# Performance work log

Measured on AMD Instinct MI355X. Metric: run time of the kernel, lower is better.

## Reference

```python
import jax, jax.numpy as jnp
import numpy as np

B, T, IN, H, OUT, L = 64, 4096, 32, 128, 32, 2


def setup_inputs() -> dict:
    key = jax.random.key(0)
    ks = jax.random.split(key, 12)
    s = 1.0 / np.sqrt(H)
    inp = {"x": jax.random.normal(ks[0], (B, T, IN), dtype=jnp.float32)}
    # layer 0 (input_dim -> H), layer 1 (H -> H); PyTorch GRU layout: [3H, in] with gates (r, z, n)
    inp["W_ih0"] = jax.random.uniform(ks[1], (3 * H, IN), jnp.float32, -s, s)
    inp["W_hh0"] = jax.random.uniform(ks[2], (3 * H, H), jnp.float32, -s, s)
    inp["b_ih0"] = jax.random.uniform(ks[3], (3 * H,), jnp.float32, -s, s)
    inp["b_hh0"] = jax.random.uniform(ks[4], (3 * H,), jnp.float32, -s, s)
    inp["W_ih1"] = jax.random.uniform(ks[5], (3 * H, H), jnp.float32, -s, s)
    inp["W_hh1"] = jax.random.uniform(ks[6], (3 * H, H), jnp.float32, -s, s)
    inp["b_ih1"] = jax.random.uniform(ks[7], (3 * H,), jnp.float32, -s, s)
    inp["b_hh1"] = jax.random.uniform(ks[8], (3 * H,), jnp.float32, -s, s)
    inp["fc_w"] = jax.random.uniform(ks[9], (OUT, H), jnp.float32, -s, s)
    inp["fc_b"] = jax.random.uniform(ks[10], (OUT,), jnp.float32, -s, s)
    return inp


def _gru_layer(x_seq, W_ih, W_hh, b_ih, b_hh):
    # x_seq: [B, T, in]; precompute the input projection as one big GEMM
    gi = jnp.einsum("bti,gi->btg", x_seq, W_ih) + b_ih  # [B, T, 3H]
    h0 = jnp.zeros((x_seq.shape[0], W_hh.shape[1]), x_seq.dtype)

    def step(h, gi_t):
        gh = h @ W_hh.T + b_hh  # [B, 3H]
        i_r, i_z, i_n = jnp.split(gi_t, 3, axis=-1)
        h_r, h_z, h_n = jnp.split(gh, 3, axis=-1)
        r = jax.nn.sigmoid(i_r + h_r)
        z = jax.nn.sigmoid(i_z + h_z)
        n = jnp.tanh(i_n + r * h_n)
        h_new = (1.0 - z) * n + z * h
        return h_new, h_new

    hT, outs = jax.lax.scan(step, h0, jnp.swapaxes(gi, 0, 1))  # outs: [T, B, H]
    return jnp.swapaxes(outs, 0, 1), hT


def reference(x, W_ih0, W_hh0, b_ih0, b_hh0, W_ih1, W_hh1, b_ih1, b_hh1, fc_w, fc_b):
    y0, h0 = _gru_layer(x, W_ih0, W_hh0, b_ih0, b_hh0)
    y1, h1 = _gru_layer(y0, W_ih1, W_hh1, b_ih1, b_hh1)
    out = jnp.einsum("bth,oh->bto", y1, fc_w) + fc_b  # [B, T, OUT]
    h = jnp.stack([h0, h1], axis=0)  # [n_layers, B, H]
    return out, h
```

## Files before the change

kernel.cpp:

```cpp
#include <hip/hip_runtime.h>

#define BB 64
#define TT 4096
#define IN0 32
#define HH 128
#define G3 384
#define NOUT 32
#define RING 64
#define CH 8

typedef _Float16 h2 __attribute__((ext_vector_type(2)));
typedef _Float16 h8 __attribute__((ext_vector_type(8)));
union H8 { h8 v; h2 p[4]; };

struct SM {
    float pg[G3 * 5];
    float pgi[G3 * 5];
    float hs[2][HH];
    _Float16 hf[2][HH];
    _Float16 xh[2][IN0];
    _Float16 ys[CH][HH];
    float bias1[G3];
    float bias2[G3];
    float fcw[NOUT * 129];
    float fcb[NOUT];
    float pfc[NOUT * 9];
};

__device__ __forceinline__ float fast_sigmoid(float x) {
    x = fminf(fmaxf(x, -30.f), 30.f);
    float e = __expf(-x);
    return __builtin_amdgcn_rcpf(1.f + e);
}
__device__ __forceinline__ float fast_tanh(float x) {
    x = fminf(fmaxf(x, -15.f), 15.f);
    float e = __expf(-2.f * x);
    return (1.f - e) * __builtin_amdgcn_rcpf(1.f + e);
}
__device__ __forceinline__ float fdot2(h2 a, h2 b, float c) {
#if __has_builtin(__builtin_amdgcn_fdot2)
    return __builtin_amdgcn_fdot2(a, b, c, false);
#else
    return fmaf((float)a.x, (float)b.x, fmaf((float)a.y, (float)b.y, c));
#endif
}
__device__ __forceinline__ int aload(const int* p) {
    return __hip_atomic_load(p, __ATOMIC_RELAXED, __HIP_MEMORY_SCOPE_AGENT);
}
__device__ __forceinline__ void astore(int* p, int v) {
    __hip_atomic_store(p, v, __ATOMIC_RELAXED, __HIP_MEMORY_SCOPE_AGENT);
}
__device__ __forceinline__ h2 cvt2(float a, float b) {
    h2 r; r.x = (_Float16)a; r.y = (_Float16)b; return r;
}

__device__ void role_A(SM& sm, const float* __restrict__ xb,
                       const float* __restrict__ W_ih, const float* __restrict__ W_hh,
                       const float* __restrict__ b_ih, const float* __restrict__ b_hh,
                       _Float16* __restrict__ y0b, float* __restrict__ hout, int* flagA)
{
    const int tid = threadIdx.x;
    const int rp = tid % 192, kq = tid / 192;
    const int r0 = 2 * rp, r1 = r0 + 1;
    const int pA0 = r0 * 5 + kq, pA1 = r1 * 5 + kq;

    h2 wh0[16], wh1[16], wi0[4], wi1[4];
    #pragma unroll
    for (int i = 0; i < 16; ++i) {
        float2 f0 = *(const float2*)&W_hh[r0 * HH + kq * 32 + 2 * i];
        float2 f1 = *(const float2*)&W_hh[r1 * HH + kq * 32 + 2 * i];
        wh0[i] = cvt2(f0.x, f0.y); wh1[i] = cvt2(f1.x, f1.y);
    }
    #pragma unroll
    for (int i = 0; i < 4; ++i) {
        float2 f0 = *(const float2*)&W_ih[r0 * IN0 + kq * 8 + 2 * i];
        float2 f1 = *(const float2*)&W_ih[r1 * IN0 + kq * 8 + 2 * i];
        wi0[i] = cvt2(f0.x, f0.y); wi1[i] = cvt2(f1.x, f1.y);
    }
    for (int i = tid; i < G3; i += 768) { sm.bias1[i] = b_ih[i]; sm.bias2[i] = b_hh[i]; }
    if (tid < HH) { sm.hs[0][tid] = 0.f; sm.hf[0][tid] = (_Float16)0.f; }
    if (tid < 8) {
        float4 f = ((const float4*)xb)[tid];
        ((h2*)&sm.xh[0][0])[2 * tid]     = cvt2(f.x, f.y);
        ((h2*)&sm.xh[0][0])[2 * tid + 1] = cvt2(f.z, f.w);
    }
    __syncthreads();

    int cur = 0;
    for (int t = 0; t < TT; ++t) {
        float4 pf;
        if (tid >= 128 && tid < 136) {
            int tn = (t + 1 < TT) ? t + 1 : t;
            pf = ((const float4*)(xb + (size_t)tn * IN0))[tid - 128];
        }
        const h8* hv = (const h8*)&sm.hf[cur][kq * 32];
        float a0 = 0.f, a1 = 0.f;
        #pragma unroll
        for (int i = 0; i < 4; ++i) {
            H8 hh; hh.v = hv[i];
            #pragma unroll
            for (int j = 0; j < 4; ++j) {
                a0 = fdot2(wh0[4 * i + j], hh.p[j], a0);
                a1 = fdot2(wh1[4 * i + j], hh.p[j], a1);
            }
        }
        sm.pg[pA0] = a0; sm.pg[pA1] = a1;
        H8 xx; xx.v = ((const h8*)&sm.xh[cur][0])[kq];
        float c0 = 0.f, c1 = 0.f;
        #pragma unroll
        for (int j = 0; j < 4; ++j) {
            c0 = fdot2(wi0[j], xx.p[j], c0);
            c1 = fdot2(wi1[j], xx.p[j], c1);
        }
        sm.pgi[pA0] = c0; sm.pgi[pA1] = c1;
        __syncthreads();

        const int nxt = cur ^ 1;
        if (tid < HH) {
            const int j = tid;
            float gir = sm.pgi[j*5+0]+sm.pgi[j*5+1]+sm.pgi[j*5+2]+sm.pgi[j*5+3] + sm.bias1[j];
            float giz = sm.pgi[(j+HH)*5+0]+sm.pgi[(j+HH)*5+1]+sm.pgi[(j+HH)*5+2]+sm.pgi[(j+HH)*5+3] + sm.bias1[j+HH];
            float gin = sm.pgi[(j+2*HH)*5+0]+sm.pgi[(j+2*HH)*5+1]+sm.pgi[(j+2*HH)*5+2]+sm.pgi[(j+2*HH)*5+3] + sm.bias1[j+2*HH];
            float ghr = sm.pg[j*5+0]+sm.pg[j*5+1]+sm.pg[j*5+2]+sm.pg[j*5+3] + sm.bias2[j];
            float ghz = sm.pg[(j+HH)*5+0]+sm.pg[(j+HH)*5+1]+sm.pg[(j+HH)*5+2]+sm.pg[(j+HH)*5+3] + sm.bias2[j+HH];
            float ghn = sm.pg[(j+2*HH)*5+0]+sm.pg[(j+2*HH)*5+1]+sm.pg[(j+2*HH)*5+2]+sm.pg[(j+2*HH)*5+3] + sm.bias2[j+2*HH];
            float rg = fast_sigmoid(gir + ghr);
            float zg = fast_sigmoid(giz + ghz);
            float ng = fast_tanh(gin + rg * ghn);
            float hn = (1.f - zg) * ng + zg * sm.hs[cur][j];
            sm.hs[nxt][j] = hn;
            sm.hf[nxt][j] = (_Float16)hn;
            y0b[(size_t)t * HH + j] = (_Float16)hn;
            if (t == TT - 1) hout[j] = hn;
        } else if (tid < 136) {
            int i = tid - 128;
            ((h2*)&sm.xh[nxt][0])[2 * i]     = cvt2(pf.x, pf.y);
            ((h2*)&sm.xh[nxt][0])[2 * i + 1] = cvt2(pf.z, pf.w);
        }
        __syncthreads();
        if ((t & 7) == 7 && tid == 0) { __threadfence(); astore(flagA, t + 1); }
        cur = nxt;
    }
}

__device__ void role_B(SM& sm, const _Float16* __restrict__ y0b,
                       const float* __restrict__ W_ih, const float* __restrict__ b_ih,
                       float* __restrict__ ring, int* flagA, int* flagB, int* flagC)
{
    const int tid = threadIdx.x;
    const int rp = tid % 192, kq = tid / 192;
    const int r0 = 2 * rp, r1 = r0 + 1;
    const int pA0 = r0 * 5 + kq, pA1 = r1 * 5 + kq;

    h2 wi0[16], wi1[16];
    #pragma unroll
    for (int i = 0; i < 16; ++i) {
        float2 f0 = *(const float2*)&W_ih[r0 * HH + kq * 32 + 2 * i];
        float2 f1 = *(const float2*)&W_ih[r1 * HH + kq * 32 + 2 * i];
        wi0[i] = cvt2(f0.x, f0.y); wi1[i] = cvt2(f1.x, f1.y);
    }
    for (int i = tid; i < G3; i += 768) sm.bias1[i] = b_ih[i];

    for (int T0 = 0; T0 < TT; T0 += CH) {
        if (tid == 0) {
            while (aload(flagA) < T0 + CH) __builtin_amdgcn_s_sleep(2);
            int need = T0 + CH - RING;
            while (aload(flagC) < need) __builtin_amdgcn_s_sleep(2);
            __threadfence();
        }
        __syncthreads();
        for (int i = tid; i < CH * HH / 2; i += 768)
            ((unsigned*)sm.ys)[i] = ((const unsigned*)(y0b + (size_t)T0 * HH))[i];
        __syncthreads();
        for (int s = 0; s < CH; ++s) {
            const h8* yv = (const h8*)&sm.ys[s][kq * 32];
            float a0 = 0.f, a1 = 0.f;
            #pragma unroll
            for (int i = 0; i < 4; ++i) {
                H8 yy; yy.v = yv[i];
                #pragma unroll
                for (int j = 0; j < 4; ++j) {
                    a0 = fdot2(wi0[4 * i + j], yy.p[j], a0);
                    a1 = fdot2(wi1[4 * i + j], yy.p[j], a1);
                }
            }
            sm.pg[pA0] = a0; sm.pg[pA1] = a1;
            __syncthreads();
            if (tid < G3) {
                float sum = sm.pg[tid*5+0]+sm.pg[tid*5+1]+sm.pg[tid*5+2]+sm.pg[tid*5+3] + sm.bias1[tid];
                ring[(size_t)((T0 + s) & (RING - 1)) * G3 + tid] = sum;
            }
            __syncthreads();
        }
        if (tid == 0) { __threadfence(); astore(flagB, T0 + CH); }
    }
}

__device__ void role_C(SM& sm, const float* __restrict__ ring,
                       const float* __restrict__ W_hh, const float* __restrict__ b_hh,
                       const float* __restrict__ fc_w, const float* __restrict__ fc_b,
                       float* __restrict__ outb, float* __restrict__ hout,
                       int* flagB, int* flagC)
{
    const int tid = threadIdx.x;
    const int rp = tid % 192, kq = tid / 192;
    const int r0 = 2 * rp, r1 = r0 + 1;
    const int pA0 = r0 * 5 + kq, pA1 = r1 * 5 + kq;

    h2 wh0[16], wh1[16];
    #pragma unroll
    for (int i = 0; i < 16; ++i) {
        float2 f0 = *(const float2*)&W_hh[r0 * HH + kq * 32 + 2 * i];
        float2 f1 = *(const float2*)&W_hh[r1 * HH + kq * 32 + 2 * i];
        wh0[i] = cvt2(f0.x, f0.y); wh1[i] = cvt2(f1.x, f1.y);
    }
    if (tid == 0) astore(flagC, 0);
    for (int i = tid; i < G3; i += 768) sm.bias2[i] = b_hh[i];
    for (int i = tid; i < NOUT * HH; i += 768)
        sm.fcw[(i >> 7) * 129 + (i & 127)] = fc_w[i];
    if (tid < NOUT) sm.fcb[tid] = fc_b[tid];
    if (tid < HH) { sm.hs[0][tid] = 0.f; sm.hf[0][tid] = (_Float16)0.f; }
    __syncthreads();

    int cur = 0;
    for (int t = 0; t < TT; ++t) {
        if ((t & 7) == 0) {
            if (tid == 0) {
                while (aload(flagB) < t + CH) __builtin_amdgcn_s_sleep(2);
                __threadfence();
            }
            __syncthreads();
        }
        if (t >= 2 && tid >= 704 && tid < 736) {
            int o = tid - 704;
            float s = sm.fcb[o];
            #pragma unroll
            for (int j = 0; j < 8; ++j) s += sm.pfc[o * 9 + j];
            outb[(size_t)(t - 2) * NOUT + o] = s;
        }
        float gir = 0.f, giz = 0.f, gin = 0.f;
        if (tid < HH) {
            const float* rr = ring + (size_t)(t & (RING - 1)) * G3;
            gir = rr[tid]; giz = rr[tid + HH]; gin = rr[tid + 2 * HH];
        }
        const h8* hv = (const h8*)&sm.hf[cur][kq * 32];
        float a0 = 0.f, a1 = 0.f;
        #pragma unroll
        for (int i = 0; i < 4; ++i) {
            H8 hh; hh.v = hv[i];
            #pragma unroll
            for (int j = 0; j < 4; ++j) {
                a0 = fdot2(wh0[4 * i + j], hh.p[j], a0);
                a1 = fdot2(wh1[4 * i + j], hh.p[j], a1);
            }
        }
        sm.pg[pA0] = a0; sm.pg[pA1] = a1;
        __syncthreads();

        const int nxt = cur ^ 1;
        if (tid < HH) {
            const int j = tid;
            float ghr = sm.pg[j*5+0]+sm.pg[j*5+1]+sm.pg[j*5+2]+sm.pg[j*5+3] + sm.bias2[j];
            float ghz = sm.pg[(j+HH)*5+0]+sm.pg[(j+HH)*5+1]+sm.pg[(j+HH)*5+2]+sm.pg[(j+HH)*5+3] + sm.bias2[j+HH];
            float ghn = sm.pg[(j+2*HH)*5+0]+sm.pg[(j+2*HH)*5+1]+sm.pg[(j+2*HH)*5+2]+sm.pg[(j+2*HH)*5+3] + sm.bias2[j+2*HH];
            float rg = fast_sigmoid(gir + ghr);
            float zg = fast_sigmoid(giz + ghz);
            float ng = fast_tanh(gin + rg * ghn);
            float hn = (1.f - zg) * ng + zg * sm.hs[cur][j];
            sm.hs[nxt][j] = hn;
            sm.hf[nxt][j] = (_Float16)hn;
            if (t == TT - 1) hout[j] = hn;
        }
        if (tid >= 384 && tid < 640) {
            int idx = tid - 384, o = idx & 31, ks = idx >> 5;
            const float* hv2 = &sm.hs[cur][ks * 16];
            const float* wv = &sm.fcw[o * 129 + ks * 16];
            float s = 0.f;
            #pragma unroll
            for (int i = 0; i < 16; ++i) s = fmaf(hv2[i], wv[i], s);
            sm.pfc[o * 9 + ks] = s;
        }
        __syncthreads();
        if ((t & 7) == 7 && tid == 0) { __threadfence(); astore(flagC, t + 1); }
        cur = nxt;
    }
    if (tid >= 704 && tid < 736) {
        int o = tid - 704;
        float s = sm.fcb[o];
        #pragma unroll
        for (int j = 0; j < 8; ++j) s += sm.pfc[o * 9 + j];
        outb[(size_t)(TT - 2) * NOUT + o] = s;
    }
    __syncthreads();
    if (tid >= 384 && tid < 640) {
        int idx = tid - 384, o = idx & 31, ks = idx >> 5;
        const float* hv2 = &sm.hs[cur][ks * 16];
        const float* wv = &sm.fcw[o * 129 + ks * 16];
        float s = 0.f;
        #pragma unroll
        for (int i = 0; i < 16; ++i) s = fmaf(hv2[i], wv[i], s);
        sm.pfc[o * 9 + ks] = s;
    }
    __syncthreads();
    if (tid >= 704 && tid < 736) {
        int o = tid - 704;
        float s = sm.fcb[o];
        #pragma unroll
        for (int j = 0; j < 8; ++j) s += sm.pfc[o * 9 + j];
        outb[(size_t)(TT - 1) * NOUT + o] = s;
    }
}

extern "C" __global__ void __launch_bounds__(768, 3)
gru_pipe_kernel(
    const float* x,
    const float* W_ih0, const float* W_hh0, const float* b_ih0, const float* b_hh0,
    const float* W_ih1, const float* W_hh1, const float* b_ih1, const float* b_hh1,
    const float* fc_w, const float* fc_b,
    float* out, float* hstack, _Float16* y0, float* ring, int* flags)
{
    __shared__ SM sm;
    const int wg = blockIdx.x;
    if (wg < BB) {
        const int b = wg;
        role_A(sm, x + (size_t)b * TT * IN0, W_ih0, W_hh0, b_ih0, b_hh0,
               y0 + (size_t)b * TT * HH, hstack + b * HH,
               &flags[(0 * 64 + b) * 16]);
    } else if (wg < 2 * BB) {
        const int b = wg - BB;
        role_B(sm, y0 + (size_t)b * TT * HH, W_ih1, b_ih1,
               ring + (size_t)b * RING * G3,
               &flags[(0 * 64 + b) * 16], &flags[(1 * 64 + b) * 16], &flags[(2 * 64 + b) * 16]);
    } else {
        const int b = wg - 2 * BB;
        role_C(sm, ring + (size_t)b * RING * G3, W_hh1, b_hh1, fc_w, fc_b,
               out + (size_t)b * TT * NOUT, hstack + BB * HH + b * HH,
               &flags[(1 * 64 + b) * 16], &flags[(2 * 64 + b) * 16]);
    }
}

extern "C" void kernel_launch(void* const* d_in, const int* in_sizes, int n_in,
                              void* d_out, int out_size, void* d_ws, size_t ws_size,
                              hipStream_t stream) {
    const float* x     = (const float*)d_in[0];
    const float* W_ih0 = (const float*)d_in[1];
    const float* W_hh0 = (const float*)d_in[2];
    const float* b_ih0 = (const float*)d_in[3];
    const float* b_hh0 = (const float*)d_in[4];
    const float* W_ih1 = (const float*)d_in[5];
    const float* W_hh1 = (const float*)d_in[6];
    const float* b_ih1 = (const float*)d_in[7];
    const float* b_hh1 = (const float*)d_in[8];
    const float* fc_w  = (const float*)d_in[9];
    const float* fc_b  = (const float*)d_in[10];

    float* out    = (float*)d_out;
    float* hstack = out + (size_t)BB * TT * NOUT;
    _Float16* y0  = (_Float16*)d_ws;
    float* ring   = (float*)((char*)d_ws + (68ull << 20));
    int* flags    = (int*)((char*)d_ws + (80ull << 20));

    gru_pipe_kernel<<<3 * BB, 768, 0, stream>>>(
        x, W_ih0, W_hh0, b_ih0, b_hh0,
        W_ih1, W_hh1, b_ih1, b_hh1,
        fc_w, fc_b, out, hstack, y0, ring, flags);
}
```

Baseline: 4.901 ms.

## Fuse both GRU layers and FC into one workgroup per batch with wavefront-skewed steps

Replaces the three-role inter-workgroup pipeline, which passed data through global memory with flag spin-waits, with a single workgroup per batch element. That workgroup runs layer 0, layer 1 and the FC projection skewed by one timestep each. Partial dot products are reduced across the four k-quarter lanes with DPP moves instead of shared-memory partial arrays, and x is prefetched in chunks of 16 steps. This removes the global y0 and ring traffic and the flag polling, but each thread now holds roughly three times as many weight registers and the workgroup does more work per step.

Result: slower. 5.779 ms (+17.9%).

```diff
diff --git a/kernel.cpp b/kernel.cpp
--- a/kernel.cpp
+++ b/kernel.cpp
@@ -6,22 +6,22 @@
 #define HH 128
 #define G3 384
 #define NOUT 32
-#define RING 64
-#define CH 8
+#define CHX 16
 
 typedef _Float16 h2 __attribute__((ext_vector_type(2)));
 typedef _Float16 h8 __attribute__((ext_vector_type(8)));
 union H8 { h8 v; h2 p[4]; };
 
 struct SM {
-    float pg[G3 * 5];
-    float pgi[G3 * 5];
-    float hs[2][HH];
-    _Float16 hf[2][HH];
-    _Float16 xh[2][IN0];
-    _Float16 ys[CH][HH];
-    float bias1[G3];
-    float bias2[G3];
+    float g0h[G3];
+    float g0i[G3];
+    float g1h[G3];
+    float g1i[G3];
+    float hs0[2][HH];
+    float hs1[2][HH];
+    _Float16 hf0[2][HH];
+    _Float16 hf1[2][HH];
+    _Float16 xh[2][CHX][IN0];
     float fcw[NOUT * 129];
     float fcb[NOUT];
     float pfc[NOUT * 9];
@@ -44,298 +44,174 @@
     return fmaf((float)a.x, (float)b.x, fmaf((float)a.y, (float)b.y, c));
 #endif
 }
-__device__ __forceinline__ int aload(const int* p) {
-    return __hip_atomic_load(p, __ATOMIC_RELAXED, __HIP_MEMORY_SCOPE_AGENT);
-}
-__device__ __forceinline__ void astore(int* p, int v) {
-    __hip_atomic_store(p, v, __ATOMIC_RELAXED, __HIP_MEMORY_SCOPE_AGENT);
-}
 __device__ __forceinline__ h2 cvt2(float a, float b) {
     h2 r; r.x = (_Float16)a; r.y = (_Float16)b; return r;
 }
-
-__device__ void role_A(SM& sm, const float* __restrict__ xb,
-                       const float* __restrict__ W_ih, const float* __restrict__ W_hh,
-                       const float* __restrict__ b_ih, const float* __restrict__ b_hh,
-                       _Float16* __restrict__ y0b, float* __restrict__ hout, int* flagA)
+__device__ __forceinline__ float qxor1(float v) {
+    return __int_as_float(__builtin_amdgcn_mov_dpp(__float_as_int(v), 0xB1, 0xF, 0xF, true));
+}
+__device__ __forceinline__ float qxor2(float v) {
+    return __int_as_float(__builtin_amdgcn_mov_dpp(__float_as_int(v), 0x4E, 0xF, 0xF, true));
+}
+
+extern "C" __global__ void __launch_bounds__(768, 3)
+gru_fused_kernel(
+    const float* __restrict__ x,
+    const float* __restrict__ W_ih0, const float* __restrict__ W_hh0,
+    const float* __restrict__ b_ih0, const float* __restrict__ b_hh0,
+    const float* __restrict__ W_ih1, const float* __restrict__ W_hh1,
+    const float* __restrict__ b_ih1, const float* __restrict__ b_hh1,
+    const float* __restrict__ fc_w, const float* __restrict__ fc_b,
+    float* __restrict__ out, float* __restrict__ hstack)
 {
+    __shared__ SM sm;
+    const int b = blockIdx.x;
     const int tid = threadIdx.x;
-    const int rp = tid % 192, kq = tid / 192;
+    const int rp = tid >> 2, kq = tid & 3;
     const int r0 = 2 * rp, r1 = r0 + 1;
-    const int pA0 = r0 * 5 + kq, pA1 = r1 * 5 + kq;
-
-    h2 wh0[16], wh1[16], wi0[4], wi1[4];
+    const float* xb = x + (size_t)b * TT * IN0;
+    float* outb = out + (size_t)b * TT * NOUT;
+
+    h2 wh0[32], wh1[32], wi1[32], wi0[8];
     #pragma unroll
     for (int i = 0; i < 16; ++i) {
-        float2 f0 = *(const float2*)&W_hh[r0 * HH + kq * 32 + 2 * i];
-        float2 f1 = *(const float2*)&W_hh[r1 * HH + kq * 32 + 2 * i];
-        wh0[i] = cvt2(f0.x, f0.y); wh1[i] = cvt2(f1.x, f1.y);
+        float2 f;
+        f = *(const float2*)&W_hh0[r0*HH + kq*32 + 2*i]; wh0[i]    = cvt2(f.x, f.y);
+        f = *(const float2*)&W_hh0[r1*HH + kq*32 + 2*i]; wh0[16+i] = cvt2(f.x, f.y);
+        f = *(const float2*)&W_hh1[r0*HH + kq*32 + 2*i]; wh1[i]    = cvt2(f.x, f.y);
+        f = *(const float2*)&W_hh1[r1*HH + kq*32 + 2*i]; wh1[16+i] = cvt2(f.x, f.y);
+        f = *(const float2*)&W_ih1[r0*HH + kq*32 + 2*i]; wi1[i]    = cvt2(f.x, f.y);
+        f = *(const float2*)&W_ih1[r1*HH + kq*32 + 2*i]; wi1[16+i] = cvt2(f.x, f.y);
     }
     #pragma unroll
     for (int i = 0; i < 4; ++i) {
-        float2 f0 = *(const float2*)&W_ih[r0 * IN0 + kq * 8 + 2 * i];
-        float2 f1 = *(const float2*)&W_ih[r1 * IN0 + kq * 8 + 2 * i];
-        wi0[i] = cvt2(f0.x, f0.y); wi1[i] = cvt2(f1.x, f1.y);
-    }
-    for (int i = tid; i < G3; i += 768) { sm.bias1[i] = b_ih[i]; sm.bias2[i] = b_hh[i]; }
-    if (tid < HH) { sm.hs[0][tid] = 0.f; sm.hf[0][tid] = (_Float16)0.f; }
-    if (tid < 8) {
-        float4 f = ((const float4*)xb)[tid];
-        ((h2*)&sm.xh[0][0])[2 * tid]     = cvt2(f.x, f.y);
-        ((h2*)&sm.xh[0][0])[2 * tid + 1] = cvt2(f.z, f.w);
-    }
-    __syncthreads();
-
-    int cur = 0;
-    for (int t = 0; t < TT; ++t) {
-        float4 pf;
-        if (tid >= 128 && tid < 136) {
-            int tn = (t + 1 < TT) ? t + 1 : t;
-            pf = ((const float4*)(xb + (size_t)tn * IN0))[tid - 128];
-        }
-        const h8* hv = (const h8*)&sm.hf[cur][kq * 32];
-        float a0 = 0.f, a1 = 0.f;
-        #pragma unroll
-        for (int i = 0; i < 4; ++i) {
-            H8 hh; hh.v = hv[i];
-            #pragma unroll
-            for (int j = 0; j < 4; ++j) {
-                a0 = fdot2(wh0[4 * i + j], hh.p[j], a0);
-                a1 = fdot2(wh1[4 * i + j], hh.p[j], a1);
-            }
-        }
-        sm.pg[pA0] = a0; sm.pg[pA1] = a1;
-        H8 xx; xx.v = ((const h8*)&sm.xh[cur][0])[kq];
-        float c0 = 0.f, c1 = 0.f;
-        #pragma unroll
-        for (int j = 0; j < 4; ++j) {
-            c0 = fdot2(wi0[j], xx.p[j], c0);
-            c1 = fdot2(wi1[j], xx.p[j], c1);
-        }
-        sm.pgi[pA0] = c0; sm.pgi[pA1] = c1;
-        __syncthreads();
-
-        const int nxt = cur ^ 1;
-        if (tid < HH) {
-            const int j = tid;
-            float gir = sm.pgi[j*5+0]+sm.pgi[j*5+1]+sm.pgi[j*5+2]+sm.pgi[j*5+3] + sm.bias1[j];
-            float giz = sm.pgi[(j+HH)*5+0]+sm.pgi[(j+HH)*5+1]+sm.pgi[(j+HH)*5+2]+sm.pgi[(j+HH)*5+3] + sm.bias1[j+HH];
-            float gin = sm.pgi[(j+2*HH)*5+0]+sm.pgi[(j+2*HH)*5+1]+sm.pgi[(j+2*HH)*5+2]+sm.pgi[(j+2*HH)*5+3] + sm.bias1[j+2*HH];
-            float ghr = sm.pg[j*5+0]+sm.pg[j*5+1]+sm.pg[j*5+2]+sm.pg[j*5+3] + sm.bias2[j];
-            float ghz = sm.pg[(j+HH)*5+0]+sm.pg[(j+HH)*5+1]+sm.pg[(j+HH)*5+2]+sm.pg[(j+HH)*5+3] + sm.bias2[j+HH];
-            float ghn = sm.pg[(j+2*HH)*5+0]+sm.pg[(j+2*HH)*5+1]+sm.pg[(j+2*HH)*5+2]+sm.pg[(j+2*HH)*5+3] + sm.bias2[j+2*HH];
-            float rg = fast_sigmoid(gir + ghr);
-            float zg = fast_sigmoid(giz + ghz);
-            float ng = fast_tanh(gin + rg * ghn);
-            float hn = (1.f - zg) * ng + zg * sm.hs[cur][j];
-            sm.hs[nxt][j] = hn;
-            sm.hf[nxt][j] = (_Float16)hn;
-            y0b[(size_t)t * HH + j] = (_Float16)hn;
-            if (t == TT - 1) hout[j] = hn;
-        } else if (tid < 136) {
-            int i = tid - 128;
-            ((h2*)&sm.xh[nxt][0])[2 * i]     = cvt2(pf.x, pf.y);
-            ((h2*)&sm.xh[nxt][0])[2 * i + 1] = cvt2(pf.z, pf.w);
-        }
-        __syncthreads();
-        if ((t & 7) == 7 && tid == 0) { __threadfence(); astore(flagA, t + 1); }
-        cur = nxt;
-    }
-}
-
-__device__ void role_B(SM& sm, const _Float16* __restrict__ y0b,
-                       const float* __restrict__ W_ih, const float* __restrict__ b_ih,
-                       float* __restrict__ ring, int* flagA, int* flagB, int* flagC)
-{
-    const int tid = threadIdx.x;
-    const int rp = tid % 192, kq = tid / 192;
-    const int r0 = 2 * rp, r1 = r0 + 1;
-    const int pA0 = r0 * 5 + kq, pA1 = r1 * 5 + kq;
-
-    h2 wi0[16], wi1[16];
-    #pragma unroll
-    for (int i = 0; i < 16; ++i) {
-        float2 f0 = *(const float2*)&W_ih[r0 * HH + kq * 32 + 2 * i];
-        float2 f1 = *(const float2*)&W_ih[r1 * HH + kq * 32 + 2 * i];
-        wi0[i] = cvt2(f0.x, f0.y); wi1[i] = cvt2(f1.x, f1.y);
-    }
-    for (int i = tid; i < G3; i += 768) sm.bias1[i] = b_ih[i];
-
-    for (int T0 = 0; T0 < TT; T0 += CH) {
-        if (tid == 0) {
-            while (aload(flagA) < T0 + CH) __builtin_amdgcn_s_sleep(2);
-            int need = T0 + CH - RING;
-            while (aload(flagC) < need) __builtin_amdgcn_s_sleep(2);
-            __threadfence();
-        }
-        __syncthreads();
-        for (int i = tid; i < CH * HH / 2; i += 768)
-            ((unsigned*)sm.ys)[i] = ((const unsigned*)(y0b + (size_t)T0 * HH))[i];
-        __syncthreads();
-        for (int s = 0; s < CH; ++s) {
-            const h8* yv = (const h8*)&sm.ys[s][kq * 32];
-            float a0 = 0.f, a1 = 0.f;
-            #pragma unroll
-            for (int i = 0; i < 4; ++i) {
-                H8 yy; yy.v = yv[i];
-                #pragma unroll
-                for (int j = 0; j < 4; ++j) {
-                    a0 = fdot2(wi0[4 * i + j], yy.p[j], a0);
-                    a1 = fdot2(wi1[4 * i + j], yy.p[j], a1);
-                }
-            }
-            sm.pg[pA0] = a0; sm.pg[pA1] = a1;
-            __syncthreads();
-            if (tid < G3) {
-                float sum = sm.pg[tid*5+0]+sm.pg[tid*5+1]+sm.pg[tid*5+2]+sm.pg[tid*5+3] + sm.bias1[tid];
-                ring[(size_t)((T0 + s) & (RING - 1)) * G3 + tid] = sum;
-            }
-            __syncthreads();
-        }
-        if (tid == 0) { __threadfence(); astore(flagB, T0 + CH); }
-    }
-}
-
-__device__ void role_C(SM& sm, const float* __restrict__ ring,
-                       const float* __restrict__ W_hh, const float* __restrict__ b_hh,
-                       const float* __restrict__ fc_w, const float* __restrict__ fc_b,
-                       float* __restrict__ outb, float* __restrict__ hout,
-                       int* flagB, int* flagC)
-{
-    const int tid = threadIdx.x;
-    const int rp = tid % 192, kq = tid / 192;
-    const int r0 = 2 * rp, r1 = r0 + 1;
-    const int pA0 = r0 * 5 + kq, pA1 = r1 * 5 + kq;
-
-    h2 wh0[16], wh1[16];
-    #pragma unroll
-    for (int i = 0; i < 16; ++i) {
-        float2 f0 = *(const float2*)&W_hh[r0 * HH + kq * 32 + 2 * i];
-        float2 f1 = *(const float2*)&W_hh[r1 * HH + kq * 32 + 2 * i];
-        wh0[i] = cvt2(f0.x, f0.y); wh1[i] = cvt2(f1.x, f1.y);
-    }
-    if (tid == 0) astore(flagC, 0);
-    for (int i = tid; i < G3; i += 768) sm.bias2[i] = b_hh[i];
+        float2 f;
+        f = *(const float2*)&W_ih0[r0*IN0 + kq*8 + 2*i]; wi0[i]   = cvt2(f.x, f.y);
+        f = *(const float2*)&W_ih0[r1*IN0 + kq*8 + 2*i]; wi0[4+i] = cvt2(f.x, f.y);
+    }
+    const bool lead = (kq == 0);
+    const float bh0a = lead ? b_hh0[r0] : 0.f, bh0b = lead ? b_hh0[r1] : 0.f;
+    const float bh1a = lead ? b_hh1[r0] : 0.f, bh1b = lead ? b_hh1[r1] : 0.f;
+    const float bi1a = lead ? b_ih1[r0] : 0.f, bi1b = lead ? b_ih1[r1] : 0.f;
+    const float bi0a = lead ? b_ih0[r0] : 0.f, bi0b = lead ? b_ih0[r1] : 0.f;
+
+    if (tid < HH) {
+        sm.hs0[0][tid] = 0.f; sm.hs0[1][tid] = 0.f;
+        sm.hs1[0][tid] = 0.f; sm.hs1[1][tid] = 0.f;
+        sm.hf0[0][tid] = (_Float16)0.f; sm.hf0[1][tid] = (_Float16)0.f;
+        sm.hf1[0][tid] = (_Float16)0.f; sm.hf1[1][tid] = (_Float16)0.f;
+    }
     for (int i = tid; i < NOUT * HH; i += 768)
         sm.fcw[(i >> 7) * 129 + (i & 127)] = fc_w[i];
     if (tid < NOUT) sm.fcb[tid] = fc_b[tid];
-    if (tid < HH) { sm.hs[0][tid] = 0.f; sm.hf[0][tid] = (_Float16)0.f; }
+    if (tid >= 640) {
+        int i = tid - 640;
+        float4 f = ((const float4*)xb)[i];
+        ((h2*)&sm.xh[0][0][0])[2*i]   = cvt2(f.x, f.y);
+        ((h2*)&sm.xh[0][0][0])[2*i+1] = cvt2(f.z, f.w);
+    }
     __syncthreads();
 
     int cur = 0;
-    for (int t = 0; t < TT; ++t) {
-        if ((t & 7) == 0) {
-            if (tid == 0) {
-                while (aload(flagB) < t + CH) __builtin_amdgcn_s_sleep(2);
-                __threadfence();
-            }
-            __syncthreads();
-        }
-        if (t >= 2 && tid >= 704 && tid < 736) {
-            int o = tid - 704;
-            float s = sm.fcb[o];
+    float4 pf;
+    for (int s = 0; s <= TT + 2; ++s) {
+        const int nxt = cur ^ 1;
+        if (tid >= 640 && (s & (CHX - 1)) == 0 && s + CHX < TT) {
+            pf = ((const float4*)(xb + (size_t)(s + CHX) * IN0))[tid - 640];
+        }
+        if (s <= TT) {
+            const h8* hv0 = (const h8*)&sm.hf0[cur][kq * 32];
+            const h8* hv1 = (const h8*)&sm.hf1[cur][kq * 32];
+            float g0h_0 = bh0a, g0h_1 = bh0b;
+            float g1h_0 = bh1a, g1h_1 = bh1b;
+            float g1i_0 = bi1a, g1i_1 = bi1b;
+            float g0i_0 = bi0a, g0i_1 = bi0b;
             #pragma unroll
-            for (int j = 0; j < 8; ++j) s += sm.pfc[o * 9 + j];
-            outb[(size_t)(t - 2) * NOUT + o] = s;
-        }
-        float gir = 0.f, giz = 0.f, gin = 0.f;
+            for (int i = 0; i < 4; ++i) {
+                H8 h0c; h0c.v = hv0[i];
+                H8 h1c; h1c.v = hv1[i];
+                #pragma unroll
+                for (int j = 0; j < 4; ++j) {
+                    const int w = 4 * i + j;
+                    g0h_0 = fdot2(wh0[w],      h0c.p[j], g0h_0);
+                    g0h_1 = fdot2(wh0[16 + w], h0c.p[j], g0h_1);
+                    g1i_0 = fdot2(wi1[w],      h0c.p[j], g1i_0);
+                    g1i_1 = fdot2(wi1[16 + w], h0c.p[j], g1i_1);
+                    g1h_0 = fdot2(wh1[w],      h1c.p[j], g1h_0);
+                    g1h_1 = fdot2(wh1[16 + w], h1c.p[j], g1h_1);
+                }
+            }
+            {
+                H8 xc; xc.v = *(const h8*)&sm.xh[(s >> 4) & 1][s & 15][kq * 8];
+                #pragma unroll
+                for (int j = 0; j < 4; ++j) {
+                    g0i_0 = fdot2(wi0[j],     xc.p[j], g0i_0);
+                    g0i_1 = fdot2(wi0[4 + j], xc.p[j], g0i_1);
+                }
+            }
+            g0h_0 += qxor1(g0h_0); g0h_0 += qxor2(g0h_0);
+            g0h_1 += qxor1(g0h_1); g0h_1 += qxor2(g0h_1);
+            g1h_0 += qxor1(g1h_0); g1h_0 += qxor2(g1h_0);
+            g1h_1 += qxor1(g1h_1); g1h_1 += qxor2(g1h_1);
+            g1i_0 += qxor1(g1i_0); g1i_0 += qxor2(g1i_0);
+            g1i_1 += qxor1(g1i_1); g1i_1 += qxor2(g1i_1);
+            g0i_0 += qxor1(g0i_0); g0i_0 += qxor2(g0i_0);
+            g0i_1 += qxor1(g0i_1); g0i_1 += qxor2(g0i_1);
+            if (kq == 0)      { *(float2*)&sm.g0h[r0] = make_float2(g0h_0, g0h_1); }
+            else if (kq == 1) { *(float2*)&sm.g1h[r0] = make_float2(g1h_0, g1h_1); }
+            else if (kq == 2) { *(float2*)&sm.g1i[r0] = make_float2(g1i_0, g1i_1); }
+            else              { *(float2*)&sm.g0i[r0] = make_float2(g0i_0, g0i_1); }
+        }
+        if (tid >= 704 && tid < 736 && s >= 3) {
+            const int o = tid - 704;
+            float sum = sm.fcb[o];
+            #pragma unroll
+            for (int j2 = 0; j2 < 8; ++j2) sum += sm.pfc[o * 9 + j2];
+            outb[(size_t)(s - 3) * NOUT + o] = sum;
+        }
+        __syncthreads();
         if (tid < HH) {
-            const float* rr = ring + (size_t)(t & (RING - 1)) * G3;
-            gir = rr[tid]; giz = rr[tid + HH]; gin = rr[tid + 2 * HH];
-        }
-        const h8* hv = (const h8*)&sm.hf[cur][kq * 32];
-        float a0 = 0.f, a1 = 0.f;
-        #pragma unroll
-        for (int i = 0; i < 4; ++i) {
-            H8 hh; hh.v = hv[i];
-            #pragma unroll
-            for (int j = 0; j < 4; ++j) {
-                a0 = fdot2(wh0[4 * i + j], hh.p[j], a0);
-                a1 = fdot2(wh1[4 * i + j], hh.p[j], a1);
-            }
-        }
-        sm.pg[pA0] = a0; sm.pg[pA1] = a1;
+            if (s < TT) {
+                const int j = tid;
+                float rg = fast_sigmoid(sm.g0i[j] + sm.g0h[j]);
+                float zg = fast_sigmoid(sm.g0i[j + HH] + sm.g0h[j + HH]);
+                float ng = fast_tanh(sm.g0i[j + 2 * HH] + rg * sm.g0h[j + 2 * HH]);
+                float hn = (1.f - zg) * ng + zg * sm.hs0[cur][j];
+                sm.hs0[nxt][j] = hn;
+                sm.hf0[nxt][j] = (_Float16)hn;
+                if (s == TT - 1) hstack[(size_t)b * HH + j] = hn;
+            }
+        } else if (tid < 2 * HH) {
+            if (s >= 1 && s <= TT) {
+                const int j = tid - HH;
+                float rg = fast_sigmoid(sm.g1i[j] + sm.g1h[j]);
+                float zg = fast_sigmoid(sm.g1i[j + HH] + sm.g1h[j + HH]);
+                float ng = fast_tanh(sm.g1i[j + 2 * HH] + rg * sm.g1h[j + 2 * HH]);
+                float hn = (1.f - zg) * ng + zg * sm.hs1[cur][j];
+                sm.hs1[nxt][j] = hn;
+                sm.hf1[nxt][j] = (_Float16)hn;
+                if (s == TT) hstack[(size_t)(BB + b) * HH + j] = hn;
+            }
+        } else if (tid >= 384 && tid < 640) {
+            if (s >= 2 && s <= TT + 1) {
+                const int idx = tid - 384, o = idx & 31, ks = idx >> 5;
+                const float* hv2 = &sm.hs1[cur][ks * 16];
+                const float* wv = &sm.fcw[o * 129 + ks * 16];
+                float ssum = 0.f;
+                #pragma unroll
+                for (int i2 = 0; i2 < 16; ++i2) ssum = fmaf(hv2[i2], wv[i2], ssum);
+                sm.pfc[o * 9 + ks] = ssum;
+            }
+        } else if (tid >= 640) {
+            if ((s & (CHX - 1)) == 7 && s + CHX - 7 < TT) {
+                const int i = tid - 640;
+                const int buf = ((s >> 4) & 1) ^ 1;
+                ((h2*)&sm.xh[buf][0][0])[2*i]   = cvt2(pf.x, pf.y);
+                ((h2*)&sm.xh[buf][0][0])[2*i+1] = cvt2(pf.z, pf.w);
+            }
+        }
         __syncthreads();
-
-        const int nxt = cur ^ 1;
-        if (tid < HH) {
-            const int j = tid;
-            float ghr = sm.pg[j*5+0]+sm.pg[j*5+1]+sm.pg[j*5+2]+sm.pg[j*5+3] + sm.bias2[j];
-            float ghz = sm.pg[(j+HH)*5+0]+sm.pg[(j+HH)*5+1]+sm.pg[(j+HH)*5+2]+sm.pg[(j+HH)*5+3] + sm.bias2[j+HH];
-            float ghn = sm.pg[(j+2*HH)*5+0]+sm.pg[(j+2*HH)*5+1]+sm.pg[(j+2*HH)*5+2]+sm.pg[(j+2*HH)*5+3] + sm.bias2[j+2*HH];
-            float rg = fast_sigmoid(gir + ghr);
-            float zg = fast_sigmoid(giz + ghz);
-            float ng = fast_tanh(gin + rg * ghn);
-            float hn = (1.f - zg) * ng + zg * sm.hs[cur][j];
-            sm.hs[nxt][j] = hn;
-            sm.hf[nxt][j] = (_Float16)hn;
-            if (t == TT - 1) hout[j] = hn;
-        }
-        if (tid >= 384 && tid < 640) {
-            int idx = tid - 384, o = idx & 31, ks = idx >> 5;
-            const float* hv2 = &sm.hs[cur][ks * 16];
-            const float* wv = &sm.fcw[o * 129 + ks * 16];
-            float s = 0.f;
-            #pragma unroll
-            for (int i = 0; i < 16; ++i) s = fmaf(hv2[i], wv[i], s);
-            sm.pfc[o * 9 + ks] = s;
-        }
-        __syncthreads();
-        if ((t & 7) == 7 && tid == 0) { __threadfence(); astore(flagC, t + 1); }
         cur = nxt;
-    }
-    if (tid >= 704 && tid < 736) {
-        int o = tid - 704;
-        float s = sm.fcb[o];
-        #pragma unroll
-        for (int j = 0; j < 8; ++j) s += sm.pfc[o * 9 + j];
-        outb[(size_t)(TT - 2) * NOUT + o] = s;
-    }
-    __syncthreads();
-    if (tid >= 384 && tid < 640) {
-        int idx = tid - 384, o = idx & 31, ks = idx >> 5;
-        const float* hv2 = &sm.hs[cur][ks * 16];
-        const float* wv = &sm.fcw[o * 129 + ks * 16];
-        float s = 0.f;
-        #pragma unroll
-        for (int i = 0; i < 16; ++i) s = fmaf(hv2[i], wv[i], s);
-        sm.pfc[o * 9 + ks] = s;
-    }
-    __syncthreads();
-    if (tid >= 704 && tid < 736) {
-        int o = tid - 704;
-        float s = sm.fcb[o];
-        #pragma unroll
-        for (int j = 0; j < 8; ++j) s += sm.pfc[o * 9 + j];
-        outb[(size_t)(TT - 1) * NOUT + o] = s;
-    }
-}
-
-extern "C" __global__ void __launch_bounds__(768, 3)
-gru_pipe_kernel(
-    const float* x,
-    const float* W_ih0, const float* W_hh0, const float* b_ih0, const float* b_hh0,
-    const float* W_ih1, const float* W_hh1, const float* b_ih1, const float* b_hh1,
-    const float* fc_w, const float* fc_b,
-    float* out, float* hstack, _Float16* y0, float* ring, int* flags)
-{
-    __shared__ SM sm;
-    const int wg = blockIdx.x;
-    if (wg < BB) {
-        const int b = wg;
-        role_A(sm, x + (size_t)b * TT * IN0, W_ih0, W_hh0, b_ih0, b_hh0,
-               y0 + (size_t)b * TT * HH, hstack + b * HH,
-               &flags[(0 * 64 + b) * 16]);
-    } else if (wg < 2 * BB) {
-        const int b = wg - BB;
-        role_B(sm, y0 + (size_t)b * TT * HH, W_ih1, b_ih1,
-               ring + (size_t)b * RING * G3,
-               &flags[(0 * 64 + b) * 16], &flags[(1 * 64 + b) * 16], &flags[(2 * 64 + b) * 16]);
-    } else {
-        const int b = wg - 2 * BB;
-        role_C(sm, ring + (size_t)b * RING * G3, W_hh1, b_hh1, fc_w, fc_b,
-               out + (size_t)b * TT * NOUT, hstack + BB * HH + b * HH,
-               &flags[(1 * 64 + b) * 16], &flags[(2 * 64 + b) * 16]);
     }
 }
 
@@ -356,12 +232,9 @@
 
     float* out    = (float*)d_out;
     float* hstack = out + (size_t)BB * TT * NOUT;
-    _Float16* y0  = (_Float16*)d_ws;
-    float* ring   = (float*)((char*)d_ws + (68ull << 20));
-    int* flags    = (int*)((char*)d_ws + (80ull << 20));
-
-    gru_pipe_kernel<<<3 * BB, 768, 0, stream>>>(
+
+    gru_fused_kernel<<<BB, 768, 0, stream>>>(
         x, W_ih0, W_hh0, b_ih0, b_hh0,
         W_ih1, W_hh1, b_ih1, b_hh1,
-        fc_w, fc_b, out, hstack, y0, ring, flags);
-}
+        fc_w, fc_b, out, hstack);
+}
```
